# Kernel optimization log

Measured on AMD Instinct MI355X. Metric: run time of the kernel, lower is better.

The kernel has to match this reference:

```python
import jax, jax.numpy as jnp
import numpy as np

N_UE = 100000
N_AP = 10000
N_E = 1600000
D = 64
H = 128


def setup_inputs() -> dict:
    key = jax.random.key(0)
    ks = jax.random.split(key, 10)
    s = 0.05
    return {
        "ue_hid": jax.random.normal(ks[0], (N_UE, D), jnp.float32),
        "ap_hid": jax.random.normal(ks[1], (N_AP, D), jnp.float32),
        "edge_hid": jax.random.normal(ks[2], (N_E, D), jnp.float32),
        "src": jax.random.randint(ks[3], (N_E,), 0, N_UE),
        "dst": jax.random.randint(ks[4], (N_E,), 0, N_AP),
        "W1a": jax.random.normal(ks[5], (2 * D, H), jnp.float32) * s,
        "b1a": jnp.zeros((H,), jnp.float32),
        "W1b": jax.random.normal(ks[6], (H, H), jnp.float32) * s,
        "b1b": jnp.zeros((H,), jnp.float32),
        "W2a": jax.random.normal(ks[7], (D + H, H), jnp.float32) * s,
        "b2a": jnp.zeros((H,), jnp.float32),
        "W2b": jax.random.normal(ks[8], (H, D), jnp.float32) * s,
        "b2b": jnp.zeros((D,), jnp.float32),
    }


def reference(ue_hid, ap_hid, edge_hid, src, dst,
              W1a, b1a, W1b, b1b, W2a, b2a, W2b, b2b):
    # message: concat(edge_feature, src UE feature) -> [E, 2D]
    msg = jnp.concatenate([edge_hid, ue_hid[src]], axis=-1)
    # mlp1 applied per edge (DGL applies it inside reduce on the mailbox,
    # which is equivalent to per-edge application followed by segment sum)
    h = jnp.maximum(msg @ W1a + b1a, 0.0) @ W1b + b1b          # [E, H]
    # sum over mailbox (all edges with the same destination AP)
    agg = jax.ops.segment_sum(h, dst, num_segments=N_AP)        # [N_AP, H]
    # mlp2 on concat(AP hid, aggregated messages)
    z = jnp.concatenate([ap_hid, agg], axis=-1)                 # [N_AP, D+H]
    new_ap = jnp.maximum(z @ W2a + b2a, 0.0) @ W2b + b2b        # [N_AP, D]
    return new_ap
```

## Files before the change

kernel.cpp:

```cpp
#include <hip/hip_runtime.h>
#include <hip/hip_bf16.h>

#define N_UE 100000
#define N_AP 10000
#define N_E  1600000
#define DD   64
#define HH   128

typedef float f32x4 __attribute__((ext_vector_type(4)));
typedef short s8b   __attribute__((ext_vector_type(8)));
typedef short s4b   __attribute__((ext_vector_type(4)));

static __device__ __forceinline__ unsigned short f2bf(float x) {
  union { float f; unsigned int u; } v; v.f = x;
  unsigned int r = v.u + 0x7fffu + ((v.u >> 16) & 1u);
  return (unsigned short)(r >> 16);
}
static __device__ __forceinline__ float bf2f(unsigned short b) {
  union { unsigned int u; float f; } v; v.u = ((unsigned int)b) << 16;
  return v.f;
}

__global__ void apk0_prep(const float* __restrict__ W1a, short* __restrict__ WTg,
                          int* __restrict__ counts) {
  int i = blockIdx.x * 256 + threadIdx.x;
  int n = gridDim.x * 256;
  for (int x = i; x < 128 * 64; x += n) {
    int col = x >> 6, k = x & 63;
    WTg[x] = (short)f2bf(W1a[k * 128 + col]);
  }
  for (int x = i; x < N_AP; x += n) counts[x] = 0;
}

__global__ __launch_bounds__(256) void apk1_ueproj(
    const float* __restrict__ ue_hid, const float* __restrict__ W1a,
    const float* __restrict__ b1a, unsigned short* __restrict__ U) {
  __shared__ float rows[16][64];
  int t = threadIdx.x;
  int base = blockIdx.x * 16;
  {
    int r = t >> 4, seg = t & 15;
    ((float4*)&rows[r][seg * 4])[0] =
        ((const float4*)(ue_hid + (size_t)(base + r) * 64))[seg];
  }
  __syncthreads();
  int j = t & 127, half = t >> 7;
  float acc[8] = {0, 0, 0, 0, 0, 0, 0, 0};
  for (int k = 0; k < 64; k++) {
    float w = W1a[(64 + k) * 128 + j];
    for (int r = 0; r < 8; r++) acc[r] += rows[half * 8 + r][k] * w;
  }
  float bb = b1a[j];
  for (int r = 0; r < 8; r++)
    U[(size_t)(base + half * 8 + r) * 128 + j] = f2bf(acc[r] + bb);
}

__global__ void apk2_hist(const int* __restrict__ dst, int* __restrict__ counts) {
  int i = blockIdx.x * blockDim.x + threadIdx.x;
  int stride = gridDim.x * blockDim.x;
  for (; i < N_E; i += stride) atomicAdd(&counts[dst[i]], 1);
}

__global__ __launch_bounds__(256) void apk3_scan(const int* __restrict__ counts,
                                                 int* __restrict__ offsets,
                                                 int* __restrict__ cursor) {
  __shared__ int p[256];
  int t = threadIdx.x;
  const int CH = 40;
  int start = t * CH, end = min(start + CH, N_AP);
  int s = 0;
  for (int i = start; i < end; i++) s += counts[i];
  p[t] = s;
  __syncthreads();
  for (int d = 1; d < 256; d <<= 1) {
    int v = p[t] + ((t >= d) ? p[t - d] : 0);
    __syncthreads();
    p[t] = v;
    __syncthreads();
  }
  int base = (t == 0) ? 0 : p[t - 1];
  for (int i = start; i < end; i++) {
    offsets[i] = base;
    cursor[i] = base;
    base += counts[i];
  }
  if (t == 255) offsets[N_AP] = base;
}

__global__ void apk4_scatter(const int* __restrict__ dst, const int* __restrict__ src,
                             int* __restrict__ cursor, int* __restrict__ order,
                             int* __restrict__ srcs) {
  int i = blockIdx.x * blockDim.x + threadIdx.x;
  int stride = gridDim.x * blockDim.x;
  for (; i < N_E; i += stride) {
    int d = dst[i];
    int pos = atomicAdd(&cursor[d], 1);
    order[pos] = i;
    srcs[pos] = src[i];
  }
}

__global__ __launch_bounds__(256) void apk5_edges(
    const float* __restrict__ edge_hid, const unsigned short* __restrict__ U,
    const short* __restrict__ WTg, const int* __restrict__ offsets,
    const int* __restrict__ order, const int* __restrict__ srcs,
    float* __restrict__ aggW) {
  __shared__ short WT[128][72];
  __shared__ short Ae[16][72];
  __shared__ unsigned short Ub[16][136];
  __shared__ int eids[16];
  __shared__ int esrc[16];
  int t = threadIdx.x;
  int a = blockIdx.x;
  int wave = t >> 6, lane = t & 63;
  int quad = lane >> 4, l16 = lane & 15;
  for (int i = t; i < 1024; i += 256) {
    int n = i >> 3, seg = i & 7;
    *(s8b*)&WT[n][seg * 8] = ((const s8b*)WTg)[i];
  }
  int start = offsets[a], end = offsets[a + 1];
  float accs0[4] = {0, 0, 0, 0}, accs1[4] = {0, 0, 0, 0};
  int col0 = wave * 32, col1 = wave * 32 + 16;
  for (int c = start; c < end; c += 16) {
    int nv = end - c; if (nv > 16) nv = 16;
    __syncthreads();
    if (t < 16) {
      int valid = (t < nv);
      eids[t] = valid ? order[c + t] : -1;
      esrc[t] = valid ? srcs[c + t] : -1;
    }
    __syncthreads();
    {
      int row = t >> 4, seg = t & 15;
      int e = eids[row];
      float4 v = make_float4(0.f, 0.f, 0.f, 0.f);
      uint4 uv = make_uint4(0u, 0u, 0u, 0u);
      if (e >= 0) {
        v  = ((const float4*)(edge_hid + (size_t)e * 64))[seg];
        uv = ((const uint4*)(U + (size_t)esrc[row] * 128))[seg];
      }
      s4b b4;
      b4[0] = (short)f2bf(v.x); b4[1] = (short)f2bf(v.y);
      b4[2] = (short)f2bf(v.z); b4[3] = (short)f2bf(v.w);
      *(s4b*)&Ae[row][seg * 4] = b4;
      *(uint4*)&Ub[row][seg * 8] = uv;
    }
    __syncthreads();
    s8b a0  = *(const s8b*)&Ae[l16][quad * 8];
    s8b a1  = *(const s8b*)&Ae[l16][32 + quad * 8];
    s8b b00 = *(const s8b*)&WT[col0 + l16][quad * 8];
    s8b b01 = *(const s8b*)&WT[col0 + l16][32 + quad * 8];
    s8b b10 = *(const s8b*)&WT[col1 + l16][quad * 8];
    s8b b11 = *(const s8b*)&WT[col1 + l16][32 + quad * 8];
    f32x4 c0 = {0.f, 0.f, 0.f, 0.f}, c1 = {0.f, 0.f, 0.f, 0.f};
    c0 = __builtin_amdgcn_mfma_f32_16x16x32_bf16(a0, b00, c0, 0, 0, 0);
    c0 = __builtin_amdgcn_mfma_f32_16x16x32_bf16(a1, b01, c0, 0, 0, 0);
    c1 = __builtin_amdgcn_mfma_f32_16x16x32_bf16(a0, b10, c1, 0, 0, 0);
    c1 = __builtin_amdgcn_mfma_f32_16x16x32_bf16(a1, b11, c1, 0, 0, 0);
    for (int r = 0; r < 4; r++) {
      int qr = quad * 4 + r;
      float u0 = bf2f(Ub[qr][col0 + l16]);
      float u1 = bf2f(Ub[qr][col1 + l16]);
      accs0[r] += fmaxf(c0[r] + u0, 0.f);
      accs1[r] += fmaxf(c1[r] + u1, 0.f);
    }
  }
  float s0 = accs0[0] + accs0[1] + accs0[2] + accs0[3];
  float s1 = accs1[0] + accs1[1] + accs1[2] + accs1[3];
  s0 += __shfl_xor(s0, 16); s0 += __shfl_xor(s0, 32);
  s1 += __shfl_xor(s1, 16); s1 += __shfl_xor(s1, 32);
  if (quad == 0) {
    aggW[(size_t)a * 128 + col0 + l16] = s0;
    aggW[(size_t)a * 128 + col1 + l16] = s1;
  }
}

__global__ __launch_bounds__(256) void apk6_mlp2(
    const float* __restrict__ ap_hid, const float* __restrict__ W1b,
    const float* __restrict__ b1b, const float* __restrict__ W2a,
    const float* __restrict__ b2a, const float* __restrict__ W2b,
    const float* __restrict__ b2b, const float* __restrict__ aggW,
    const int* __restrict__ offsets, float* __restrict__ out) {
  __shared__ float wbuf[64 * 128];
  __shared__ float zrows[16 * 128];
  __shared__ float yrows[16 * 128];
  __shared__ float arows[16 * 64];
  __shared__ float cbuf[16];
  int t = threadIdx.x;
  int apb = blockIdx.x * 16;
  for (int i = t; i < 16 * 128 / 4; i += 256)
    ((float4*)zrows)[i] = ((const float4*)(aggW + (size_t)apb * 128))[i];
  for (int i = t; i < 16 * 64 / 4; i += 256)
    ((float4*)arows)[i] = ((const float4*)(ap_hid + (size_t)apb * 64))[i];
  if (t < 16) cbuf[t] = (float)(offsets[apb + t + 1] - offsets[apb + t]);
  int j = t & 127, half = t >> 7;
  {
    float bb = b1b[j];
    __syncthreads();
    float acc[8];
    for (int r = 0; r < 8; r++) acc[r] = cbuf[half * 8 + r] * bb;
    for (int p = 0; p < 2; p++) {
      __syncthreads();
      for (int i = t; i < 64 * 128 / 4; i += 256)
        ((float4*)wbuf)[i] = ((const float4*)(W1b + p * 64 * 128))[i];
      __syncthreads();
      for (int k = 0; k < 64; k++) {
        float w = wbuf[k * 128 + j];
        for (int r = 0; r < 8; r++)
          acc[r] += zrows[(half * 8 + r) * 128 + (p * 64 + k)] * w;
      }
    }
    for (int r = 0; r < 8; r++) yrows[(half * 8 + r) * 128 + j] = acc[r];
  }
  {
    float acc2[8];
    float bb = b2a[j];
    for (int r = 0; r < 8; r++) acc2[r] = bb;
    __syncthreads();
    for (int i = t; i < 64 * 128 / 4; i += 256)
      ((float4*)wbuf)[i] = ((const float4*)W2a)[i];
    __syncthreads();
    for (int k = 0; k < 64; k++) {
      float w = wbuf[k * 128 + j];
      for (int r = 0; r < 8; r++) acc2[r] += arows[(half * 8 + r) * 64 + k] * w;
    }
    for (int p = 0; p < 2; p++) {
      __syncthreads();
      for (int i = t; i < 64 * 128 / 4; i += 256)
        ((float4*)wbuf)[i] = ((const float4*)(W2a + (64 + p * 64) * 128))[i];
      __syncthreads();
      for (int k = 0; k < 64; k++) {
        float w = wbuf[k * 128 + j];
        for (int r = 0; r < 8; r++)
          acc2[r] += yrows[(half * 8 + r) * 128 + (p * 64 + k)] * w;
      }
    }
    __syncthreads();
    for (int r = 0; r < 8; r++)
      zrows[(half * 8 + r) * 128 + j] = fmaxf(acc2[r], 0.f);
  }
  {
    __syncthreads();
    for (int i = t; i < 128 * 64 / 4; i += 256)
      ((float4*)wbuf)[i] = ((const float4*)W2b)[i];
    __syncthreads();
    int i2 = t & 63, q = t >> 6;
    float acc3[4];
    float bb = b2b[i2];
    for (int r = 0; r < 4; r++) acc3[r] = bb;
    for (int k = 0; k < 128; k++) {
      float w = wbuf[k * 64 + i2];
      for (int r = 0; r < 4; r++) acc3[r] += zrows[(q * 4 + r) * 128 + k] * w;
    }
    for (int r = 0; r < 4; r++)
      out[(size_t)(apb + q * 4 + r) * 64 + i2] = acc3[r];
  }
}

extern "C" void kernel_launch(void* const* d_in, const int* in_sizes, int n_in,
                              void* d_out, int out_size, void* d_ws, size_t ws_size,
                              hipStream_t stream) {
  const float* ue_hid   = (const float*)d_in[0];
  const float* ap_hid   = (const float*)d_in[1];
  const float* edge_hid = (const float*)d_in[2];
  const int*   src      = (const int*)d_in[3];
  const int*   dst      = (const int*)d_in[4];
  const float* W1a      = (const float*)d_in[5];
  const float* b1a      = (const float*)d_in[6];
  const float* W1b      = (const float*)d_in[7];
  const float* b1b      = (const float*)d_in[8];
  const float* W2a      = (const float*)d_in[9];
  const float* b2a      = (const float*)d_in[10];
  const float* W2b      = (const float*)d_in[11];
  const float* b2b      = (const float*)d_in[12];
  float* out = (float*)d_out;

  unsigned char* ws = (unsigned char*)d_ws;
  unsigned short* U = (unsigned short*)(ws);
  short* WTg        = (short*)(ws + 25600000);
  int* counts       = (int*)(ws + 25616384);
  int* offsets      = (int*)(ws + 25656576);
  int* cursor       = (int*)(ws + 25696768);
  int* order        = (int*)(ws + 25736960);
  int* srcs         = (int*)(ws + 32136960);
  float* aggW       = (float*)(ws + 38536960);

  apk0_prep<<<40, 256, 0, stream>>>(W1a, WTg, counts);
  apk1_ueproj<<<N_UE / 16, 256, 0, stream>>>(ue_hid, W1a, b1a, U);
  apk2_hist<<<2048, 256, 0, stream>>>(dst, counts);
  apk3_scan<<<1, 256, 0, stream>>>(counts, offsets, cursor);
  apk4_scatter<<<2048, 256, 0, stream>>>(dst, src, cursor, order, srcs);
  apk5_edges<<<N_AP, 256, 0, stream>>>(edge_hid, U, WTg, offsets, order, srcs, aggW);
  apk6_mlp2<<<N_AP / 16, 256, 0, stream>>>(ap_hid, W1b, b1b, W2a, b2a, W2b, b2b,
                                           aggW, offsets, out);
}
```

Before: 930.5 us.

## Tile edges in fixed 128-edge blocks with full K=128 MFMA and atomic segment reduction

Removes the separate UE projection kernel and instead gathers raw edge and UE rows, computing the full concatenated 128-wide first-layer GEMM per 128-edge tile with MFMA. Each block handles a fixed chunk of dst-sorted edges rather than one AP, and accumulates per-segment partial sums with atomics into a zeroed aggregate buffer. Order and src indices are packed into one int4 record. This balances load across blocks and removes small 16-edge iterations with many barriers. In exchange it reads full fp32 UE rows per edge, does twice the MFMA work per edge, and adds float atomics that make summation order nondeterministic.

```diff
diff --git a/kernel.cpp b/kernel.cpp
--- a/kernel.cpp
+++ b/kernel.cpp
@@ -16,43 +16,18 @@
   unsigned int r = v.u + 0x7fffu + ((v.u >> 16) & 1u);
   return (unsigned short)(r >> 16);
 }
-static __device__ __forceinline__ float bf2f(unsigned short b) {
-  union { unsigned int u; float f; } v; v.u = ((unsigned int)b) << 16;
-  return v.f;
-}
 
 __global__ void apk0_prep(const float* __restrict__ W1a, short* __restrict__ WTg,
-                          int* __restrict__ counts) {
+                          int* __restrict__ counts, float* __restrict__ aggW) {
   int i = blockIdx.x * 256 + threadIdx.x;
   int n = gridDim.x * 256;
-  for (int x = i; x < 128 * 64; x += n) {
-    int col = x >> 6, k = x & 63;
+  for (int x = i; x < 128 * 128; x += n) {
+    int col = x >> 7, k = x & 127;
     WTg[x] = (short)f2bf(W1a[k * 128 + col]);
   }
   for (int x = i; x < N_AP; x += n) counts[x] = 0;
-}
-
-__global__ __launch_bounds__(256) void apk1_ueproj(
-    const float* __restrict__ ue_hid, const float* __restrict__ W1a,
-    const float* __restrict__ b1a, unsigned short* __restrict__ U) {
-  __shared__ float rows[16][64];
-  int t = threadIdx.x;
-  int base = blockIdx.x * 16;
-  {
-    int r = t >> 4, seg = t & 15;
-    ((float4*)&rows[r][seg * 4])[0] =
-        ((const float4*)(ue_hid + (size_t)(base + r) * 64))[seg];
-  }
-  __syncthreads();
-  int j = t & 127, half = t >> 7;
-  float acc[8] = {0, 0, 0, 0, 0, 0, 0, 0};
-  for (int k = 0; k < 64; k++) {
-    float w = W1a[(64 + k) * 128 + j];
-    for (int r = 0; r < 8; r++) acc[r] += rows[half * 8 + r][k] * w;
-  }
-  float bb = b1a[j];
-  for (int r = 0; r < 8; r++)
-    U[(size_t)(base + half * 8 + r) * 128 + j] = f2bf(acc[r] + bb);
+  for (int x = i; x < N_AP * 128 / 4; x += n)
+    ((float4*)aggW)[x] = make_float4(0.f, 0.f, 0.f, 0.f);
 }
 
 __global__ void apk2_hist(const int* __restrict__ dst, int* __restrict__ counts) {
@@ -88,90 +63,106 @@
 }
 
 __global__ void apk4_scatter(const int* __restrict__ dst, const int* __restrict__ src,
-                             int* __restrict__ cursor, int* __restrict__ order,
-                             int* __restrict__ srcs) {
+                             int* __restrict__ cursor, int4* __restrict__ triple) {
   int i = blockIdx.x * blockDim.x + threadIdx.x;
   int stride = gridDim.x * blockDim.x;
   for (; i < N_E; i += stride) {
     int d = dst[i];
     int pos = atomicAdd(&cursor[d], 1);
-    order[pos] = i;
-    srcs[pos] = src[i];
-  }
-}
-
-__global__ __launch_bounds__(256) void apk5_edges(
-    const float* __restrict__ edge_hid, const unsigned short* __restrict__ U,
-    const short* __restrict__ WTg, const int* __restrict__ offsets,
-    const int* __restrict__ order, const int* __restrict__ srcs,
-    float* __restrict__ aggW) {
-  __shared__ short WT[128][72];
-  __shared__ short Ae[16][72];
-  __shared__ unsigned short Ub[16][136];
-  __shared__ int eids[16];
-  __shared__ int esrc[16];
-  int t = threadIdx.x;
-  int a = blockIdx.x;
-  int wave = t >> 6, lane = t & 63;
-  int quad = lane >> 4, l16 = lane & 15;
-  for (int i = t; i < 1024; i += 256) {
-    int n = i >> 3, seg = i & 7;
-    *(s8b*)&WT[n][seg * 8] = ((const s8b*)WTg)[i];
-  }
-  int start = offsets[a], end = offsets[a + 1];
-  float accs0[4] = {0, 0, 0, 0}, accs1[4] = {0, 0, 0, 0};
-  int col0 = wave * 32, col1 = wave * 32 + 16;
-  for (int c = start; c < end; c += 16) {
-    int nv = end - c; if (nv > 16) nv = 16;
-    __syncthreads();
-    if (t < 16) {
-      int valid = (t < nv);
-      eids[t] = valid ? order[c + t] : -1;
-      esrc[t] = valid ? srcs[c + t] : -1;
-    }
-    __syncthreads();
-    {
-      int row = t >> 4, seg = t & 15;
-      int e = eids[row];
-      float4 v = make_float4(0.f, 0.f, 0.f, 0.f);
-      uint4 uv = make_uint4(0u, 0u, 0u, 0u);
-      if (e >= 0) {
-        v  = ((const float4*)(edge_hid + (size_t)e * 64))[seg];
-        uv = ((const uint4*)(U + (size_t)esrc[row] * 128))[seg];
+    triple[pos] = make_int4(i, src[i], d, 0);
+  }
+}
+
+__global__ __launch_bounds__(256, 2) void apk5_edges(
+    const float* __restrict__ edge_hid, const float* __restrict__ ue_hid,
+    const short* __restrict__ WTg, const float* __restrict__ b1a,
+    const int4* __restrict__ triple, float* __restrict__ aggW) {
+  __shared__ short WT[128][140];
+  __shared__ short A[128][140];
+  __shared__ int eids[128];
+  __shared__ int usrc[128];
+  __shared__ int segs[128];
+  int t = threadIdx.x, blk = blockIdx.x;
+  int wave = t >> 6, lane = t & 63, quad = lane >> 4, l16 = lane & 15;
+
+  if (t < 128) {
+    int4 tr = triple[(size_t)blk * 128 + t];
+    eids[t] = tr.x; usrc[t] = tr.y; segs[t] = tr.z;
+  }
+  for (int i = t; i < 2048; i += 256) {
+    int col = i >> 4, seg16 = i & 15;
+    *(s8b*)&WT[col][seg16 * 8] = ((const s8b*)WTg)[i];
+  }
+  __syncthreads();
+
+  {
+    int r = t >> 1, h = t & 1;
+    const float* srow = h ? (ue_hid + (size_t)usrc[r] * 64)
+                          : (edge_hid + (size_t)eids[r] * 64);
+    int kb = h * 64;
+    for (int cc = 0; cc < 8; cc++) {
+      float4 v = ((const float4*)srow)[cc * 2];
+      float4 w = ((const float4*)srow)[cc * 2 + 1];
+      s8b p;
+      p[0] = (short)f2bf(v.x); p[1] = (short)f2bf(v.y);
+      p[2] = (short)f2bf(v.z); p[3] = (short)f2bf(v.w);
+      p[4] = (short)f2bf(w.x); p[5] = (short)f2bf(w.y);
+      p[6] = (short)f2bf(w.z); p[7] = (short)f2bf(w.w);
+      *(s8b*)&A[r][kb + cc * 8] = p;
+    }
+  }
+  __syncthreads();
+
+  s8b bf[2][4];
+  for (int ct = 0; ct < 2; ct++)
+    for (int ks = 0; ks < 4; ks++)
+      bf[ct][ks] = *(const s8b*)&WT[wave * 32 + ct * 16 + l16][ks * 32 + quad * 8];
+  float bias0 = b1a[wave * 32 + l16];
+  float bias1 = b1a[wave * 32 + 16 + l16];
+
+  int runseg = segs[0];
+  float run0 = 0.f, run1 = 0.f;
+  for (int rt = 0; rt < 8; rt++) {
+    s8b a0 = *(const s8b*)&A[rt * 16 + l16][quad * 8];
+    s8b a1 = *(const s8b*)&A[rt * 16 + l16][32 + quad * 8];
+    s8b a2 = *(const s8b*)&A[rt * 16 + l16][64 + quad * 8];
+    s8b a3 = *(const s8b*)&A[rt * 16 + l16][96 + quad * 8];
+    f32x4 c0 = {0.f, 0.f, 0.f, 0.f}, c1 = {0.f, 0.f, 0.f, 0.f};
+    c0 = __builtin_amdgcn_mfma_f32_16x16x32_bf16(a0, bf[0][0], c0, 0, 0, 0);
+    c0 = __builtin_amdgcn_mfma_f32_16x16x32_bf16(a1, bf[0][1], c0, 0, 0, 0);
+    c0 = __builtin_amdgcn_mfma_f32_16x16x32_bf16(a2, bf[0][2], c0, 0, 0, 0);
+    c0 = __builtin_amdgcn_mfma_f32_16x16x32_bf16(a3, bf[0][3], c0, 0, 0, 0);
+    c1 = __builtin_amdgcn_mfma_f32_16x16x32_bf16(a0, bf[1][0], c1, 0, 0, 0);
+    c1 = __builtin_amdgcn_mfma_f32_16x16x32_bf16(a1, bf[1][1], c1, 0, 0, 0);
+    c1 = __builtin_amdgcn_mfma_f32_16x16x32_bf16(a2, bf[1][2], c1, 0, 0, 0);
+    c1 = __builtin_amdgcn_mfma_f32_16x16x32_bf16(a3, bf[1][3], c1, 0, 0, 0);
+    int sj[4]; float t0[4], t1[4];
+    for (int j = 0; j < 4; j++) {
+      int gr = rt * 16 + quad * 4 + j;
+      sj[j] = segs[gr];
+      t0[j] = fmaxf(c0[j] + bias0, 0.f);
+      t1[j] = fmaxf(c1[j] + bias1, 0.f);
+    }
+    int s0 = segs[rt * 16], s1 = segs[rt * 16 + 15];
+    for (int s = s0; s <= s1; s++) {
+      float v0 = 0.f, v1 = 0.f;
+      for (int j = 0; j < 4; j++)
+        if (sj[j] == s) { v0 += t0[j]; v1 += t1[j]; }
+      v0 += __shfl_xor(v0, 16); v0 += __shfl_xor(v0, 32);
+      v1 += __shfl_xor(v1, 16); v1 += __shfl_xor(v1, 32);
+      if (s == runseg) { run0 += v0; run1 += v1; }
+      else {
+        if (quad == 0) {
+          atomicAdd(&aggW[(size_t)runseg * 128 + wave * 32 + l16], run0);
+          atomicAdd(&aggW[(size_t)runseg * 128 + wave * 32 + 16 + l16], run1);
+        }
+        runseg = s; run0 = v0; run1 = v1;
       }
-      s4b b4;
-      b4[0] = (short)f2bf(v.x); b4[1] = (short)f2bf(v.y);
-      b4[2] = (short)f2bf(v.z); b4[3] = (short)f2bf(v.w);
-      *(s4b*)&Ae[row][seg * 4] = b4;
-      *(uint4*)&Ub[row][seg * 8] = uv;
-    }
-    __syncthreads();
-    s8b a0  = *(const s8b*)&Ae[l16][quad * 8];
-    s8b a1  = *(const s8b*)&Ae[l16][32 + quad * 8];
-    s8b b00 = *(const s8b*)&WT[col0 + l16][quad * 8];
-    s8b b01 = *(const s8b*)&WT[col0 + l16][32 + quad * 8];
-    s8b b10 = *(const s8b*)&WT[col1 + l16][quad * 8];
-    s8b b11 = *(const s8b*)&WT[col1 + l16][32 + quad * 8];
-    f32x4 c0 = {0.f, 0.f, 0.f, 0.f}, c1 = {0.f, 0.f, 0.f, 0.f};
-    c0 = __builtin_amdgcn_mfma_f32_16x16x32_bf16(a0, b00, c0, 0, 0, 0);
-    c0 = __builtin_amdgcn_mfma_f32_16x16x32_bf16(a1, b01, c0, 0, 0, 0);
-    c1 = __builtin_amdgcn_mfma_f32_16x16x32_bf16(a0, b10, c1, 0, 0, 0);
-    c1 = __builtin_amdgcn_mfma_f32_16x16x32_bf16(a1, b11, c1, 0, 0, 0);
-    for (int r = 0; r < 4; r++) {
-      int qr = quad * 4 + r;
-      float u0 = bf2f(Ub[qr][col0 + l16]);
-      float u1 = bf2f(Ub[qr][col1 + l16]);
-      accs0[r] += fmaxf(c0[r] + u0, 0.f);
-      accs1[r] += fmaxf(c1[r] + u1, 0.f);
-    }
-  }
-  float s0 = accs0[0] + accs0[1] + accs0[2] + accs0[3];
-  float s1 = accs1[0] + accs1[1] + accs1[2] + accs1[3];
-  s0 += __shfl_xor(s0, 16); s0 += __shfl_xor(s0, 32);
-  s1 += __shfl_xor(s1, 16); s1 += __shfl_xor(s1, 32);
+    }
+  }
   if (quad == 0) {
-    aggW[(size_t)a * 128 + col0 + l16] = s0;
-    aggW[(size_t)a * 128 + col1 + l16] = s1;
+    atomicAdd(&aggW[(size_t)runseg * 128 + wave * 32 + l16], run0);
+    atomicAdd(&aggW[(size_t)runseg * 128 + wave * 32 + 16 + l16], run1);
   }
 }
 
@@ -276,21 +267,18 @@
   float* out = (float*)d_out;
 
   unsigned char* ws = (unsigned char*)d_ws;
-  unsigned short* U = (unsigned short*)(ws);
-  short* WTg        = (short*)(ws + 25600000);
-  int* counts       = (int*)(ws + 25616384);
-  int* offsets      = (int*)(ws + 25656576);
-  int* cursor       = (int*)(ws + 25696768);
-  int* order        = (int*)(ws + 25736960);
-  int* srcs         = (int*)(ws + 32136960);
-  float* aggW       = (float*)(ws + 38536960);
-
-  apk0_prep<<<40, 256, 0, stream>>>(W1a, WTg, counts);
-  apk1_ueproj<<<N_UE / 16, 256, 0, stream>>>(ue_hid, W1a, b1a, U);
+  short* WTg    = (short*)(ws);
+  int* counts   = (int*)(ws + 32768);
+  int* offsets  = (int*)(ws + 73728);
+  int* cursor   = (int*)(ws + 114688);
+  float* aggW   = (float*)(ws + 155648);
+  int4* triple  = (int4*)(ws + 5275648);
+
+  apk0_prep<<<640, 256, 0, stream>>>(W1a, WTg, counts, aggW);
   apk2_hist<<<2048, 256, 0, stream>>>(dst, counts);
   apk3_scan<<<1, 256, 0, stream>>>(counts, offsets, cursor);
-  apk4_scatter<<<2048, 256, 0, stream>>>(dst, src, cursor, order, srcs);
-  apk5_edges<<<N_AP, 256, 0, stream>>>(edge_hid, U, WTg, offsets, order, srcs, aggW);
+  apk4_scatter<<<2048, 256, 0, stream>>>(dst, src, cursor, triple);
+  apk5_edges<<<N_E / 128, 256, 0, stream>>>(edge_hid, ue_hid, WTg, b1a, triple, aggW);
   apk6_mlp2<<<N_AP / 16, 256, 0, stream>>>(ap_hid, W1b, b1b, W2a, b2a, W2b, b2b,
                                            aggW, offsets, out);
 }
```

Measured after the change: 947.3 us. About the same (+1.8%).
